# Optimization experiments

Hardware: AMD Instinct MI355X
Metric: run time of the kernel (lower is better)

The kernel has to match this reference:

```python
import jax, jax.numpy as jnp
import numpy as np

VOCAB = 32000
DIM = 1024
DFF = 4096
NLLM = 3
B, S = 2, 2048
THRESH = 0.98
EPS = 1e-8


def setup_inputs() -> dict:
    key = jax.random.key(0)
    ks = jax.random.split(key, 5)
    x = jax.random.randint(ks[0], (B, S), 0, VOCAB)
    emb = 0.02 * jax.random.normal(ks[1], (VOCAB, DIM), jnp.float32)
    ln_g = jnp.ones((NLLM, DIM), jnp.float32)
    ln_b = jnp.zeros((NLLM, DIM), jnp.float32)
    W1 = 0.002 * jax.random.normal(ks[2], (NLLM, DIM, DFF), jnp.float32)
    b1 = jnp.zeros((NLLM, DFF), jnp.float32)
    W2 = 0.002 * jax.random.normal(ks[3], (NLLM, DFF, DIM), jnp.float32)
    b2 = jnp.zeros((NLLM, DIM), jnp.float32)
    W_out = (1.0 / np.sqrt(DIM)) * jax.random.normal(ks[4], (VOCAB, DIM), jnp.float32)
    return dict(x=x, emb=emb, ln_g=ln_g, ln_b=ln_b, W1=W1, b1=b1, W2=W2, b2=b2, W_out=W_out)


def _layernorm(h, g, b):
    m = jnp.mean(h, axis=-1, keepdims=True)
    v = jnp.var(h, axis=-1, keepdims=True)
    return (h - m) * jax.lax.rsqrt(v + 1e-5) * g + b


def reference(x, emb, ln_g, ln_b, W1, b1, W2, b2, W_out):
    # Cascaded early-exit ensemble. The torch code physically re-packs surviving
    # tokens; since each LLM block here is per-token (residual MLP), a masked
    # formulation computes identical per-token math and is jit-compatible.
    Bb, Ss = x.shape
    T = Bb * Ss
    h = emb[x.reshape(T)]                      # [T, D] token embeddings
    active = jnp.ones((T,), dtype=bool)
    final = jnp.zeros((T, VOCAB), dtype=h.dtype)
    for i in range(NLLM):                      # fixed, small number of LLMs
        hn = _layernorm(h, ln_g[i], ln_b[i])
        mlp = jax.nn.gelu(hn @ W1[i] + b1[i]) @ W2[i] + b2[i]
        h_out = h + mlp                        # [T, D]
        logits = h_out @ W_out.T               # [T, V] shared output head
        cos = jnp.sum(h * h_out, axis=-1) / (
            jnp.linalg.norm(h, axis=-1) * jnp.linalg.norm(h_out, axis=-1) + EPS)
        is_last = (i == NLLM - 1)
        should_exit = cos >= THRESH
        take = active if is_last else (active & should_exit)
        final = jnp.where(take[:, None], logits, final)   # scatter logits for exiting tokens
        active = active & (~take)
        h = jnp.where(active[:, None], h_out, h)          # continuing tokens carry h_out forward
    return final.reshape(Bb, Ss, VOCAB)
```

## Files before the change

### kernel.cpp

```cpp
#include <hip/hip_runtime.h>
#include <hip/hip_bf16.h>
#include <stdint.h>

constexpr int TK   = 4096;
constexpr int DIMC = 1024;
constexpr int DFFC = 4096;
constexpr int VOC  = 32000;
constexpr int NL   = 3;

typedef __attribute__((ext_vector_type(8))) short bf16x8;
typedef __attribute__((ext_vector_type(8))) _Float16 half8;
typedef __attribute__((ext_vector_type(4))) float f32x4;
using u16 = unsigned short;

__device__ __forceinline__ u16 f2bf(float f) {
  unsigned int u = __float_as_uint(f);
  u += 0x7FFF + ((u >> 16) & 1);
  return (u16)(u >> 16);
}

__device__ __forceinline__ void split16(float v, u16& hi, u16& lo) {
  _Float16 a = (_Float16)v;
  _Float16 b = (_Float16)(v - (float)a);
  hi = __builtin_bit_cast(u16, a);
  lo = __builtin_bit_cast(u16, b);
}

__device__ __forceinline__ float gelu_f(float x) {
  float x3 = x * x * x;
  return 0.5f * x * (1.0f + tanhf(0.7978845608028654f * (x + 0.044715f * x3)));
}

__device__ __forceinline__ void gll16(const void* g, void* l) {
  __builtin_amdgcn_global_load_lds(
      (const __attribute__((address_space(1))) unsigned int*)g,
      (__attribute__((address_space(3))) unsigned int*)l, 16, 0, 0);
}

__global__ __launch_bounds__(256) void k_init(const int* __restrict__ x,
    const float* __restrict__ emb,
    const float* __restrict__ g, const float* __restrict__ b,
    float* __restrict__ h, u16* __restrict__ hn1, u16* __restrict__ hn2,
    int* __restrict__ surv, int* __restrict__ cnts) {
  const int t = blockIdx.x, tid = threadIdx.x;
  if (t == 0 && tid < 16) cnts[tid] = (tid == 12) ? TK : 0;
  if (tid == 0) surv[t] = t;
  const int tok = x[t];
  const int lane = tid & 63, wid = tid >> 6;
  __shared__ float sm[4];
  float4 v = ((const float4*)(emb + (size_t)tok * DIMC))[tid];
  ((float4*)(h + (size_t)t * DIMC))[tid] = v;
  float s = v.x + v.y + v.z + v.w;
#pragma unroll
  for (int o = 32; o; o >>= 1) s += __shfl_down(s, o);
  if (lane == 0) sm[wid] = s;
  __syncthreads();
  const float mean = (sm[0] + sm[1] + sm[2] + sm[3]) * (1.0f / DIMC);
  __syncthreads();
  float4 d;
  d.x = v.x - mean; d.y = v.y - mean; d.z = v.z - mean; d.w = v.w - mean;
  float q = d.x * d.x + d.y * d.y + d.z * d.z + d.w * d.w;
#pragma unroll
  for (int o = 32; o; o >>= 1) q += __shfl_down(q, o);
  if (lane == 0) sm[wid] = q;
  __syncthreads();
  const float var = (sm[0] + sm[1] + sm[2] + sm[3]) * (1.0f / DIMC);
  const float rstd = 1.0f / sqrtf(var + 1e-5f);
  float4 gg = ((const float4*)g)[tid];
  float4 bb = ((const float4*)b)[tid];
  float o4[4];
  o4[0] = (d.x * rstd * gg.x + bb.x) * 16.f;
  o4[1] = (d.y * rstd * gg.y + bb.y) * 16.f;
  o4[2] = (d.z * rstd * gg.z + bb.z) * 16.f;
  o4[3] = (d.w * rstd * gg.w + bb.w) * 16.f;
  ushort4 u1, u2;
  split16(o4[0], u1.x, u2.x); split16(o4[1], u1.y, u2.y);
  split16(o4[2], u1.z, u2.z); split16(o4[3], u1.w, u2.w);
  ((ushort4*)(hn1 + (size_t)t * DIMC))[tid] = u1;
  ((ushort4*)(hn2 + (size_t)t * DIMC))[tid] = u2;
}

__global__ __launch_bounds__(256) void k_prep(
    const float* __restrict__ W1, const float* __restrict__ W2,
    u16* __restrict__ W1all, u16* __restrict__ W2all,
    const float* __restrict__ Wout, u16* __restrict__ Woutb)
{
  int bid = blockIdx.x;
  if (bid >= 6144) {
    int i = (bid - 6144) * 256 + threadIdx.x;
    const int n4 = VOC * DIMC / 4;
    const int stride = 2048 * 256;
    for (; i < n4; i += stride) {
      float4 v = ((const float4*)Wout)[i];
      ushort4 u;
      u.x = f2bf(v.x); u.y = f2bf(v.y); u.z = f2bf(v.z); u.w = f2bf(v.w);
      ((ushort4*)Woutb)[i] = u;
    }
    return;
  }
  const int s = bid >> 11; bid &= 2047;
  const int tens = bid >> 10; bid &= 1023;
  const float* W; int K, N; u16 *O1, *O2; int bk, bn;
  if (tens == 0) {
    W = W1 + (size_t)s * DIMC * DFFC; K = DIMC; N = DFFC;
    O1 = W1all + (size_t)s * 2 * DFFC * DIMC;
    O2 = O1 + (size_t)DFFC * DIMC;
    bk = (bid & 15) * 64; bn = (bid >> 4) * 64;
  } else {
    W = W2 + (size_t)s * DFFC * DIMC; K = DFFC; N = DIMC;
    O1 = W2all + (size_t)s * 2 * DIMC * DFFC;
    O2 = O1 + (size_t)DIMC * DFFC;
    bk = (bid >> 4) * 64; bn = (bid & 15) * 64;
  }
  __shared__ float t[64][65];
  const int lx = threadIdx.x & 63, ly = threadIdx.x >> 6;
#pragma unroll
  for (int i = 0; i < 64; i += 4)
    t[ly + i][lx] = W[(size_t)(bk + ly + i) * N + bn + lx];
  __syncthreads();
  const int n4 = threadIdx.x >> 4;
  const int kq = (threadIdx.x & 15) * 4;
#pragma unroll
  for (int j = 0; j < 4; ++j) {
    const int n = j * 16 + n4;
    ushort4 h1, h2;
    {
      float v0 = t[kq + 0][n] * 256.f, v1 = t[kq + 1][n] * 256.f;
      float v2 = t[kq + 2][n] * 256.f, v3 = t[kq + 3][n] * 256.f;
      split16(v0, h1.x, h2.x); split16(v1, h1.y, h2.y);
      split16(v2, h1.z, h2.z); split16(v3, h1.w, h2.w);
    }
    const size_t o = (size_t)(bn + n) * K + bk + kq;
    *(ushort4*)&O1[o] = h1;
    *(ushort4*)&O2[o] = h2;
  }
}

__global__ __launch_bounds__(512, 1) void k_mlp1(
    const u16* __restrict__ wsb,
    int offA, int pstrA,
    int offB, int pstrB,
    const int* __restrict__ pM,
    const float* __restrict__ bias,
    u16* __restrict__ O1, u16* __restrict__ O2)
{
  const int x = blockIdx.x & 7, g = blockIdx.x >> 3;
  const int rb = g & 15;
  const int cb = x * 2 + (g >> 4);
  const int M = *pM;
  if (rb * 256 >= M) return;
  const int n0 = cb * 256;

  __shared__ u16 S[2][32768];
  const int tid = threadIdx.x, w = tid >> 6, l = tid & 63;
  const int lr16 = l & 15, hi = l >> 4;

  int goff[8];
#pragma unroll
  for (int q = 0; q < 8; ++q) {
    const int bi = w * 8 + q;
    const int side = bi >> 5;
    const int pl = (bi >> 4) & 1;
    const int j = bi & 15;
    const int row = (side ? n0 : rb * 256) + j * 16 + lr16;
    const int base = side ? (offB + pl * pstrB) : (offA + pl * pstrA);
    goff[q] = base + row * DIMC + hi * 8;
  }

  const int wr = w >> 2, wc = w & 3;
  f32x4 acc[8][4];
#pragma unroll
  for (int mi = 0; mi < 8; ++mi)
#pragma unroll
    for (int ni = 0; ni < 4; ++ni) acc[mi][ni] = (f32x4){0.f, 0.f, 0.f, 0.f};

  auto STAGE = [&](int buf, int kt) {
#pragma unroll
    for (int q = 0; q < 8; ++q)
      gll16(wsb + (size_t)(goff[q] + kt * 32), (void*)&S[buf][(w * 8 + q) * 512]);
  };

  STAGE(0, 0);
  STAGE(1, 1);
  const int NT = DIMC / 32;
  for (int kt = 0; kt < NT; ++kt) {
    const int cur = kt & 1;
    if (kt + 1 < NT) asm volatile("s_waitcnt vmcnt(8)" ::: "memory");
    else             asm volatile("s_waitcnt vmcnt(0)" ::: "memory");
    __builtin_amdgcn_s_barrier();
    half8 b1v[4], b2v[4];
#pragma unroll
    for (int ni = 0; ni < 4; ++ni) {
      const int sub = (32 + wc * 4 + ni) * 512 + l * 8;
      b1v[ni] = *(const half8*)&S[cur][sub];
      b2v[ni] = *(const half8*)&S[cur][sub + 8192];
    }
#pragma unroll
    for (int mh = 0; mh < 2; ++mh) {
      half8 a1v[4], a2v[4];
#pragma unroll
      for (int i = 0; i < 4; ++i) {
        const int sub = (wr * 8 + mh * 4 + i) * 512 + l * 8;
        a1v[i] = *(const half8*)&S[cur][sub];
        a2v[i] = *(const half8*)&S[cur][sub + 8192];
      }
      __builtin_amdgcn_s_setprio(1);
#pragma unroll
      for (int i = 0; i < 4; ++i)
#pragma unroll
        for (int ni = 0; ni < 4; ++ni) {
          f32x4 c = acc[mh * 4 + i][ni];
          c = __builtin_amdgcn_mfma_f32_16x16x32_f16(a2v[i], b1v[ni], c, 0, 0, 0);
          c = __builtin_amdgcn_mfma_f32_16x16x32_f16(a1v[i], b2v[ni], c, 0, 0, 0);
          c = __builtin_amdgcn_mfma_f32_16x16x32_f16(a1v[i], b1v[ni], c, 0, 0, 0);
          acc[mh * 4 + i][ni] = c;
        }
      __builtin_amdgcn_s_setprio(0);
    }
    asm volatile("s_waitcnt lgkmcnt(0)" ::: "memory");
    __builtin_amdgcn_s_barrier();
    if (kt + 2 < NT) STAGE(cur, kt + 2);
  }

#pragma unroll
  for (int mi = 0; mi < 8; ++mi)
#pragma unroll
    for (int ni = 0; ni < 4; ++ni) {
      const int n = n0 + wc * 64 + ni * 16 + lr16;
#pragma unroll
      for (int r = 0; r < 4; ++r) {
        const int m = rb * 256 + wr * 128 + mi * 16 + hi * 4 + r;
        float v = gelu_f(acc[mi][ni][r] * (1.f / 4096.f) + bias[n]) * 64.f;
        u16 h1, h2; split16(v, h1, h2);
        O1[(size_t)m * DFFC + n] = h1;
        O2[(size_t)m * DFFC + n] = h2;
      }
    }
}

__global__ __launch_bounds__(512, 1) void k_mlp2(
    const u16* __restrict__ wsb,
    int offA, int pstrA,
    int offB, int pstrB,
    const int* __restrict__ pM,
    float* __restrict__ PO)
{
  const int x = blockIdx.x & 7, g = blockIdx.x >> 3;
  const int rb = g & 15;
  const int cz = x * 2 + (g >> 4);
  const int cb = cz & 7, z = cz >> 3;
  const int M = *pM;
  if (rb * 256 >= M) return;
  const int n0 = cb * 128;
  const int kz = z * 2048;

  __shared__ u16 S[2][24576];
  const int tid = threadIdx.x, w = tid >> 6, l = tid & 63;
  const int lr16 = l & 15, hi = l >> 4;

  int goff[6];
#pragma unroll
  for (int q = 0; q < 6; ++q) {
    const int bi = w * 6 + q;
    int base, row;
    if (bi < 32) {
      const int pl = bi >> 4, j = bi & 15;
      base = offA + pl * pstrA;
      row = rb * 256 + j * 16 + lr16;
    } else {
      const int bb = bi - 32, pl = bb >> 3, j = bb & 7;
      base = offB + pl * pstrB;
      row = n0 + j * 16 + lr16;
    }
    goff[q] = base + row * DFFC + kz + hi * 8;
  }

  const int wr = w >> 1, wc = w & 1;
  f32x4 acc[4][4];
#pragma unroll
  for (int mi = 0; mi < 4; ++mi)
#pragma unroll
    for (int ni = 0; ni < 4; ++ni) acc[mi][ni] = (f32x4){0.f, 0.f, 0.f, 0.f};

  auto STAGE = [&](int buf, int kt) {
#pragma unroll
    for (int q = 0; q < 6; ++q)
      gll16(wsb + (size_t)(goff[q] + kt * 32), (void*)&S[buf][(w * 6 + q) * 512]);
  };

  STAGE(0, 0);
  STAGE(1, 1);
  const int NT = 2048 / 32;
  for (int kt = 0; kt < NT; ++kt) {
    const int cur = kt & 1;
    if (kt + 1 < NT) asm volatile("s_waitcnt vmcnt(6)" ::: "memory");
    else             asm volatile("s_waitcnt vmcnt(0)" ::: "memory");
    __builtin_amdgcn_s_barrier();
    half8 a1v[4], a2v[4], b1v[4], b2v[4];
#pragma unroll
    for (int mi = 0; mi < 4; ++mi) {
      const int sub = (wr * 4 + mi) * 512 + l * 8;
      a1v[mi] = *(const half8*)&S[cur][sub];
      a2v[mi] = *(const half8*)&S[cur][sub + 8192];
    }
#pragma unroll
    for (int ni = 0; ni < 4; ++ni) {
      const int sub = (32 + wc * 4 + ni) * 512 + l * 8;
      b1v[ni] = *(const half8*)&S[cur][sub];
      b2v[ni] = *(const half8*)&S[cur][sub + 4096];
    }
    __builtin_amdgcn_s_setprio(1);
#pragma unroll
    for (int mi = 0; mi < 4; ++mi)
#pragma unroll
      for (int ni = 0; ni < 4; ++ni) {
        f32x4 c = acc[mi][ni];
        c = __builtin_amdgcn_mfma_f32_16x16x32_f16(a2v[mi], b1v[ni], c, 0, 0, 0);
        c = __builtin_amdgcn_mfma_f32_16x16x32_f16(a1v[mi], b2v[ni], c, 0, 0, 0);
        c = __builtin_amdgcn_mfma_f32_16x16x32_f16(a1v[mi], b1v[ni], c, 0, 0, 0);
        acc[mi][ni] = c;
      }
    __builtin_amdgcn_s_setprio(0);
    asm volatile("s_waitcnt lgkmcnt(0)" ::: "memory");
    __builtin_amdgcn_s_barrier();
    if (kt + 2 < NT) STAGE(cur, kt + 2);
  }

#pragma unroll
  for (int mi = 0; mi < 4; ++mi)
#pragma unroll
    for (int ni = 0; ni < 4; ++ni) {
      const int n = n0 + wc * 64 + ni * 16 + lr16;
#pragma unroll
      for (int r = 0; r < 4; ++r) {
        const int m = rb * 256 + wr * 64 + mi * 16 + hi * 4 + r;
        PO[(size_t)(z * TK + m) * DIMC + n] = acc[mi][ni][r] * (1.f / 16384.f);
      }
    }
}

__global__ __launch_bounds__(256) void k_decide(
    float* __restrict__ h, const float* __restrict__ p,
    const float* __restrict__ bias,
    const int* __restrict__ surv_in, int* __restrict__ surv_out,
    const int* __restrict__ pM, int* __restrict__ cnts,
    int* __restrict__ exit_idx, u16* __restrict__ hexit,
    const float* __restrict__ gnx, const float* __restrict__ bnx,
    u16* __restrict__ hn1, u16* __restrict__ hn2,
    int stage)
{
  const int bidx = blockIdx.x;
  if (bidx >= *pM) return;
  const int t = surv_in[bidx];
  const int tid = threadIdx.x;
  const int lane = tid & 63, wid = tid >> 6;
  __shared__ float sm[16];
  __shared__ int sif[2];
  float4 a  = ((const float4*)(h + (size_t)t * DIMC))[tid];
  float4 p0 = ((const float4*)(p + (size_t)bidx * DIMC))[tid];
  float4 p1 = ((const float4*)(p + (size_t)(TK + bidx) * DIMC))[tid];
  float4 bb = ((const float4*)bias)[tid];
  float4 o;
  o.x = a.x + p0.x + p1.x + bb.x;
  o.y = a.y + p0.y + p1.y + bb.y;
  o.z = a.z + p0.z + p1.z + bb.z;
  o.w = a.w + p0.w + p1.w + bb.w;
  float hh = a.x * a.x + a.y * a.y + a.z * a.z + a.w * a.w;
  float ho = a.x * o.x + a.y * o.y + a.z * o.z + a.w * o.w;
  float oo = o.x * o.x + o.y * o.y + o.z * o.z + o.w * o.w;
  float so = o.x + o.y + o.z + o.w;
#pragma unroll
  for (int off = 32; off; off >>= 1) {
    hh += __shfl_down(hh, off);
    ho += __shfl_down(ho, off);
    oo += __shfl_down(oo, off);
    so += __shfl_down(so, off);
  }
  if (lane == 0) { sm[wid] = hh; sm[4 + wid] = ho; sm[8 + wid] = oo; sm[12 + wid] = so; }
  __syncthreads();
  const float mean = (sm[12] + sm[13] + sm[14] + sm[15]) * (1.0f / DIMC);
  if (tid == 0) {
    int take;
    if (stage == NL - 1) take = 1;
    else {
      const float HH = sm[0] + sm[1] + sm[2] + sm[3];
      const float HO = sm[4] + sm[5] + sm[6] + sm[7];
      const float OO = sm[8] + sm[9] + sm[10] + sm[11];
      const float cosv = HO / (sqrtf(HH) * sqrtf(OO) + 1e-8f);
      take = (cosv >= 0.98f) ? 1 : 0;
    }
    int pos;
    if (take) {
      pos = atomicAdd(&cnts[stage], 1);
      exit_idx[pos] = t;
    } else {
      pos = atomicAdd(&cnts[4 + stage], 1);
      surv_out[pos] = t;
    }
    sif[0] = take; sif[1] = pos;
  }
  __syncthreads();
  if (sif[0]) {
    u16* dst = hexit + (size_t)sif[1] * DIMC;
    ushort4 u;
    u.x = f2bf(o.x); u.y = f2bf(o.y); u.z = f2bf(o.z); u.w = f2bf(o.w);
    ((ushort4*)dst)[tid] = u;
  } else {
    ((float4*)(h + (size_t)t * DIMC))[tid] = o;
    float4 d;
    d.x = o.x - mean; d.y = o.y - mean; d.z = o.z - mean; d.w = o.w - mean;
    float q = d.x * d.x + d.y * d.y + d.z * d.z + d.w * d.w;
#pragma unroll
    for (int off = 32; off; off >>= 1) q += __shfl_down(q, off);
    if (lane == 0) sm[wid] = q;
    __syncthreads();
    const float var = (sm[0] + sm[1] + sm[2] + sm[3]) * (1.0f / DIMC);
    const float rstd = 1.0f / sqrtf(var + 1e-5f);
    float4 gg = ((const float4*)gnx)[tid];
    float4 b2 = ((const float4*)bnx)[tid];
    float o4[4];
    o4[0] = (d.x * rstd * gg.x + b2.x) * 16.f;
    o4[1] = (d.y * rstd * gg.y + b2.y) * 16.f;
    o4[2] = (d.z * rstd * gg.z + b2.z) * 16.f;
    o4[3] = (d.w * rstd * gg.w + b2.w) * 16.f;
    ushort4 u1, u2;
    split16(o4[0], u1.x, u2.x); split16(o4[1], u1.y, u2.y);
    split16(o4[2], u1.z, u2.z); split16(o4[3], u1.w, u2.w);
    const int pos = sif[1];
    ((ushort4*)(hn1 + (size_t)pos * DIMC))[tid] = u1;
    ((ushort4*)(hn2 + (size_t)pos * DIMC))[tid] = u2;
  }
}

__global__ __launch_bounds__(512, 4) void k_logits(
    const u16* __restrict__ wsb, int offA, int offB,
    const int* __restrict__ pcnt,
    const int* __restrict__ exit_idx,
    float* __restrict__ out)
{
  const int x = blockIdx.x & 7, g = blockIdx.x >> 3;
  const int rb = g & 15;
  const int cb = x * 32 + (g >> 4);
  if (cb >= VOC / 128) return;
  const int cnt = *pcnt;
  if (rb * 256 >= cnt) return;
  const int n0 = cb * 128;

  __shared__ u16 S[2][12288];
  const int tid = threadIdx.x, w = tid >> 6, l = tid & 63;
  const int lr16 = l & 15, hi = l >> 4;

  int goff[3], loff[3];
#pragma unroll
  for (int q = 0; q < 3; ++q) {
    const int bi = w * 3 + q;
    if (bi < 16) {
      goff[q] = offA + (rb * 256 + bi * 16 + lr16) * DIMC + hi * 8;
      loff[q] = bi * 512;
    } else {
      const int j = bi - 16;
      goff[q] = offB + (n0 + j * 16 + lr16) * DIMC + hi * 8;
      loff[q] = 8192 + j * 512;
    }
  }

  const int wr = w >> 1, wc = w & 1;
  f32x4 acc[4][4];
#pragma unroll
  for (int mi = 0; mi < 4; ++mi)
#pragma unroll
    for (int ni = 0; ni < 4; ++ni) acc[mi][ni] = (f32x4){0.f, 0.f, 0.f, 0.f};

  auto STAGE = [&](int buf, int kt) {
#pragma unroll
    for (int q = 0; q < 3; ++q)
      gll16(wsb + (size_t)(goff[q] + kt * 32), (void*)&S[buf][loff[q]]);
  };

  STAGE(0, 0);
  STAGE(1, 1);
  const int NT = DIMC / 32;
  for (int kt = 0; kt < NT; ++kt) {
    const int cur = kt & 1;
    if (kt + 1 < NT) asm volatile("s_waitcnt vmcnt(3)" ::: "memory");
    else             asm volatile("s_waitcnt vmcnt(0)" ::: "memory");
    __builtin_amdgcn_s_barrier();
    bf16x8 aF[4], bF[4];
#pragma unroll
    for (int mi = 0; mi < 4; ++mi)
      aF[mi] = *(const bf16x8*)&S[cur][(wr * 4 + mi) * 512 + l * 8];
#pragma unroll
    for (int ni = 0; ni < 4; ++ni)
      bF[ni] = *(const bf16x8*)&S[cur][8192 + (wc * 4 + ni) * 512 + l * 8];
    __builtin_amdgcn_s_setprio(1);
#pragma unroll
    for (int mi = 0; mi < 4; ++mi)
#pragma unroll
      for (int ni = 0; ni < 4; ++ni)
        acc[mi][ni] = __builtin_amdgcn_mfma_f32_16x16x32_bf16(aF[mi], bF[ni], acc[mi][ni], 0, 0, 0);
    __builtin_amdgcn_s_setprio(0);
    asm volatile("s_waitcnt lgkmcnt(0)" ::: "memory");
    __builtin_amdgcn_s_barrier();
    if (kt + 2 < NT) STAGE(cur, kt + 2);
  }

  const int mvalid = cnt - rb * 256;
#pragma unroll
  for (int mi = 0; mi < 4; ++mi)
#pragma unroll
    for (int r = 0; r < 4; ++r) {
      const int mrow = wr * 64 + mi * 16 + hi * 4 + r;
      if (mrow < mvalid) {
        const int tok = exit_idx[rb * 256 + mrow];
        float* orow = out + (size_t)tok * VOC + n0 + wc * 64 + lr16;
#pragma unroll
        for (int ni = 0; ni < 4; ++ni)
          __builtin_nontemporal_store(acc[mi][ni][r], &orow[ni * 16]);
      }
    }
}

extern "C" void kernel_launch(void* const* d_in, const int* in_sizes, int n_in,
                              void* d_out, int out_size, void* d_ws, size_t ws_size,
                              hipStream_t stream)
{
  const int*   x    = (const int*)d_in[0];
  const float* emb  = (const float*)d_in[1];
  const float* ln_g = (const float*)d_in[2];
  const float* ln_b = (const float*)d_in[3];
  const float* W1   = (const float*)d_in[4];
  const float* b1   = (const float*)d_in[5];
  const float* W2   = (const float*)d_in[6];
  const float* b2   = (const float*)d_in[7];
  const float* Wout = (const float*)d_in[8];
  float* out = (float*)d_out;

  char* p = (char*)d_ws;
  size_t off = 0;
  auto alloc = [&](size_t bytes) -> void* {
    void* r = p + off;
    off += (bytes + 255) & ~(size_t)255;
    return r;
  };
  u16* wsb = (u16*)d_ws;
  float* h    = (float*)alloc((size_t)TK * DIMC * 4);
  float* pbuf = (float*)alloc((size_t)2 * TK * DIMC * 4);
  u16* hn1 = (u16*)alloc((size_t)2 * TK * DIMC * 2);
  u16* hn2 = hn1 + (size_t)TK * DIMC;
  u16* act1 = (u16*)alloc((size_t)2 * TK * DFFC * 2);
  u16* act2 = act1 + (size_t)TK * DFFC;
  u16* Woutb = (u16*)alloc((size_t)VOC * DIMC * 2);
  u16* W1all = (u16*)alloc((size_t)NL * 2 * DFFC * DIMC * 2);
  u16* W2all = (u16*)alloc((size_t)NL * 2 * DIMC * DFFC * 2);
  u16* hexit = (u16*)alloc((size_t)TK * DIMC * 2);
  int* exit_idx = (int*)alloc((size_t)TK * 4);
  int* surv_a   = (int*)alloc((size_t)TK * 4);
  int* surv_b   = (int*)alloc((size_t)TK * 4);
  int* cnts     = (int*)alloc(64 * 4);

  const int offHn  = (int)(hn1  - wsb);
  const int offAct = (int)(act1 - wsb);
  const int offWob = (int)(Woutb- wsb);
  const int offW1a = (int)(W1all- wsb);
  const int offW2a = (int)(W2all- wsb);
  const int offHex = (int)(hexit- wsb);
  const int pstrHn  = TK * DIMC;
  const int pstrAct = TK * DFFC;
  const int pstrW   = DFFC * DIMC;

  k_init<<<TK, 256, 0, stream>>>(x, emb, ln_g, ln_b, h, hn1, hn2, surv_a, cnts);
  k_prep<<<8192, 256, 0, stream>>>(W1, W2, W1all, W2all, Wout, Woutb);
  int* surv_in  = surv_a;
  int* surv_out = surv_b;
  for (int i = 0; i < NL; ++i) {
    const int* pM = (i == 0) ? (cnts + 12) : (cnts + 4 + (i - 1));
    k_mlp1<<<256, 512, 0, stream>>>(
        wsb, offHn, pstrHn, offW1a + i * 2 * pstrW, pstrW,
        pM, b1 + (size_t)i * DFFC, act1, act2);
    k_mlp2<<<256, 512, 0, stream>>>(
        wsb, offAct, pstrAct, offW2a + i * 2 * pstrW, pstrW, pM, pbuf);
    const int inx = (i + 1 < NL) ? (i + 1) : i;
    k_decide<<<TK, 256, 0, stream>>>(h, pbuf, b2 + (size_t)i * DIMC,
        surv_in, surv_out, pM, cnts, exit_idx, hexit,
        ln_g + (size_t)inx * DIMC, ln_b + (size_t)inx * DIMC, hn1, hn2, i);
    k_logits<<<4096, 512, 0, stream>>>(wsb, offHex, offWob, cnts + i, exit_idx, out);
    int* tmp = surv_in; surv_in = surv_out; surv_out = tmp;
  }
}
```

Before: 1.368 ms.

## Interleave next-tile global loads with MFMA phases in both GEMM kernels

Replaces the prefetch-two-tiles-ahead double buffer with a schedule that splits each k-step into phases. Half of the next tile's global-to-LDS loads are issued inside each early phase, interleaved with the MFMA work, and a barrier is placed after every phase. The aim is to spread memory traffic across the compute instead of bursting it at the end of each step. In exchange the prefetch distance drops to one tile, the loop waits on vmcnt(0) every iteration, and there are more barriers per step, so load latency may be exposed.

```diff
diff --git a/kernel.cpp b/kernel.cpp
--- a/kernel.cpp
+++ b/kernel.cpp
@@ -174,52 +174,52 @@
 #pragma unroll
     for (int ni = 0; ni < 4; ++ni) acc[mi][ni] = (f32x4){0.f, 0.f, 0.f, 0.f};
 
-  auto STAGE = [&](int buf, int kt) {
-#pragma unroll
-    for (int q = 0; q < 8; ++q)
+  auto STAGE_H = [&](int buf, int kt, int h4) {
+#pragma unroll
+    for (int q = h4 * 4; q < h4 * 4 + 4; ++q)
       gll16(wsb + (size_t)(goff[q] + kt * 32), (void*)&S[buf][(w * 8 + q) * 512]);
   };
 
-  STAGE(0, 0);
-  STAGE(1, 1);
+  STAGE_H(0, 0, 0); STAGE_H(0, 0, 1);
   const int NT = DIMC / 32;
   for (int kt = 0; kt < NT; ++kt) {
     const int cur = kt & 1;
-    if (kt + 1 < NT) asm volatile("s_waitcnt vmcnt(8)" ::: "memory");
-    else             asm volatile("s_waitcnt vmcnt(0)" ::: "memory");
+    asm volatile("s_waitcnt vmcnt(0)" ::: "memory");
     __builtin_amdgcn_s_barrier();
     half8 b1v[4], b2v[4];
 #pragma unroll
-    for (int ni = 0; ni < 4; ++ni) {
-      const int sub = (32 + wc * 4 + ni) * 512 + l * 8;
-      b1v[ni] = *(const half8*)&S[cur][sub];
-      b2v[ni] = *(const half8*)&S[cur][sub + 8192];
-    }
-#pragma unroll
-    for (int mh = 0; mh < 2; ++mh) {
-      half8 a1v[4], a2v[4];
-#pragma unroll
-      for (int i = 0; i < 4; ++i) {
-        const int sub = (wr * 8 + mh * 4 + i) * 512 + l * 8;
+    for (int ph = 0; ph < 4; ++ph) {
+      half8 a1v[2], a2v[2];
+      if (ph == 0) {
+#pragma unroll
+        for (int ni = 0; ni < 4; ++ni) {
+          const int sub = (32 + wc * 4 + ni) * 512 + l * 8;
+          b1v[ni] = *(const half8*)&S[cur][sub];
+          b2v[ni] = *(const half8*)&S[cur][sub + 8192];
+        }
+      }
+#pragma unroll
+      for (int i = 0; i < 2; ++i) {
+        const int sub = (wr * 8 + ph * 2 + i) * 512 + l * 8;
         a1v[i] = *(const half8*)&S[cur][sub];
         a2v[i] = *(const half8*)&S[cur][sub + 8192];
       }
+      if (ph < 2 && kt + 1 < NT) STAGE_H(cur ^ 1, kt + 1, ph);
+      asm volatile("s_waitcnt lgkmcnt(0)" ::: "memory");
       __builtin_amdgcn_s_setprio(1);
 #pragma unroll
-      for (int i = 0; i < 4; ++i)
+      for (int i = 0; i < 2; ++i)
 #pragma unroll
         for (int ni = 0; ni < 4; ++ni) {
-          f32x4 c = acc[mh * 4 + i][ni];
+          f32x4 c = acc[ph * 2 + i][ni];
           c = __builtin_amdgcn_mfma_f32_16x16x32_f16(a2v[i], b1v[ni], c, 0, 0, 0);
           c = __builtin_amdgcn_mfma_f32_16x16x32_f16(a1v[i], b2v[ni], c, 0, 0, 0);
           c = __builtin_amdgcn_mfma_f32_16x16x32_f16(a1v[i], b1v[ni], c, 0, 0, 0);
-          acc[mh * 4 + i][ni] = c;
+          acc[ph * 2 + i][ni] = c;
         }
       __builtin_amdgcn_s_setprio(0);
-    }
-    asm volatile("s_waitcnt lgkmcnt(0)" ::: "memory");
-    __builtin_amdgcn_s_barrier();
-    if (kt + 2 < NT) STAGE(cur, kt + 2);
+      __builtin_amdgcn_s_barrier();
+    }
   }
 
 #pragma unroll
@@ -282,48 +282,52 @@
 #pragma unroll
     for (int ni = 0; ni < 4; ++ni) acc[mi][ni] = (f32x4){0.f, 0.f, 0.f, 0.f};
 
-  auto STAGE = [&](int buf, int kt) {
-#pragma unroll
-    for (int q = 0; q < 6; ++q)
+  auto STAGE_H = [&](int buf, int kt, int h3) {
+#pragma unroll
+    for (int q = h3 * 3; q < h3 * 3 + 3; ++q)
       gll16(wsb + (size_t)(goff[q] + kt * 32), (void*)&S[buf][(w * 6 + q) * 512]);
   };
 
-  STAGE(0, 0);
-  STAGE(1, 1);
+  STAGE_H(0, 0, 0); STAGE_H(0, 0, 1);
   const int NT = 2048 / 32;
   for (int kt = 0; kt < NT; ++kt) {
     const int cur = kt & 1;
-    if (kt + 1 < NT) asm volatile("s_waitcnt vmcnt(6)" ::: "memory");
-    else             asm volatile("s_waitcnt vmcnt(0)" ::: "memory");
+    asm volatile("s_waitcnt vmcnt(0)" ::: "memory");
     __builtin_amdgcn_s_barrier();
-    half8 a1v[4], a2v[4], b1v[4], b2v[4];
-#pragma unroll
-    for (int mi = 0; mi < 4; ++mi) {
-      const int sub = (wr * 4 + mi) * 512 + l * 8;
-      a1v[mi] = *(const half8*)&S[cur][sub];
-      a2v[mi] = *(const half8*)&S[cur][sub + 8192];
-    }
-#pragma unroll
-    for (int ni = 0; ni < 4; ++ni) {
-      const int sub = (32 + wc * 4 + ni) * 512 + l * 8;
-      b1v[ni] = *(const half8*)&S[cur][sub];
-      b2v[ni] = *(const half8*)&S[cur][sub + 4096];
-    }
-    __builtin_amdgcn_s_setprio(1);
-#pragma unroll
-    for (int mi = 0; mi < 4; ++mi)
-#pragma unroll
-      for (int ni = 0; ni < 4; ++ni) {
-        f32x4 c = acc[mi][ni];
-        c = __builtin_amdgcn_mfma_f32_16x16x32_f16(a2v[mi], b1v[ni], c, 0, 0, 0);
-        c = __builtin_amdgcn_mfma_f32_16x16x32_f16(a1v[mi], b2v[ni], c, 0, 0, 0);
-        c = __builtin_amdgcn_mfma_f32_16x16x32_f16(a1v[mi], b1v[ni], c, 0, 0, 0);
-        acc[mi][ni] = c;
-      }
-    __builtin_amdgcn_s_setprio(0);
-    asm volatile("s_waitcnt lgkmcnt(0)" ::: "memory");
-    __builtin_amdgcn_s_barrier();
-    if (kt + 2 < NT) STAGE(cur, kt + 2);
+    half8 a1v[4], a2v[4];
+#pragma unroll
+    for (int ph = 0; ph < 2; ++ph) {
+      half8 b1v[2], b2v[2];
+      if (ph == 0) {
+#pragma unroll
+        for (int mi = 0; mi < 4; ++mi) {
+          const int sub = (wr * 4 + mi) * 512 + l * 8;
+          a1v[mi] = *(const half8*)&S[cur][sub];
+          a2v[mi] = *(const half8*)&S[cur][sub + 8192];
+        }
+      }
+#pragma unroll
+      for (int ni = 0; ni < 2; ++ni) {
+        const int sub = (32 + wc * 4 + ph * 2 + ni) * 512 + l * 8;
+        b1v[ni] = *(const half8*)&S[cur][sub];
+        b2v[ni] = *(const half8*)&S[cur][sub + 4096];
+      }
+      if (kt + 1 < NT) STAGE_H(cur ^ 1, kt + 1, ph);
+      asm volatile("s_waitcnt lgkmcnt(0)" ::: "memory");
+      __builtin_amdgcn_s_setprio(1);
+#pragma unroll
+      for (int mi = 0; mi < 4; ++mi)
+#pragma unroll
+        for (int ni = 0; ni < 2; ++ni) {
+          f32x4 c = acc[mi][ph * 2 + ni];
+          c = __builtin_amdgcn_mfma_f32_16x16x32_f16(a2v[mi], b1v[ni], c, 0, 0, 0);
+          c = __builtin_amdgcn_mfma_f32_16x16x32_f16(a1v[mi], b2v[ni], c, 0, 0, 0);
+          c = __builtin_amdgcn_mfma_f32_16x16x32_f16(a1v[mi], b1v[ni], c, 0, 0, 0);
+          acc[mi][ph * 2 + ni] = c;
+        }
+      __builtin_amdgcn_s_setprio(0);
+      __builtin_amdgcn_s_barrier();
+    }
   }
 
 #pragma unroll
```

New measurement: 1.325 ms (median of 2 runs). -3.2%, faster.
